# Kernel tuning notes

Measured on AMD Instinct MI355X. Metric: run time of the kernel, lower is better.

## Reference

```python
import jax, jax.numpy as jnp
import numpy as np

B, D, N, C = 4096, 2048, 8, 1024  # batch, in_features, ncomponents, per-component out channels


def setup_inputs() -> dict:
    key = jax.random.key(0)
    k1, k2, k3, k4 = jax.random.split(key, 4)
    scale_w = 1.0 / np.sqrt(D)
    return {
        "x": jax.random.normal(k1, (B, D), dtype=jnp.float32),
        "W": jax.random.normal(k2, (N, C, D), dtype=jnp.float32) * scale_w,
        "b": jax.random.normal(k3, (N, C), dtype=jnp.float32) * scale_w,
        "Wg_w": jax.random.normal(k4, (D, 1), dtype=jnp.float32) * scale_w,
        "Wg_b": jnp.zeros((1,), dtype=jnp.float32),
    }


def reference(x, W, b, Wg_w, Wg_b):
    n = W.shape[0]
    # scalar gate per sample: g in [0, ncomponents]
    g = n * 0.5 * (1.0 + jnp.tanh(x @ Wg_w + Wg_b))            # [B, 1]
    k = jnp.floor(g)                                            # [B, 1]
    idx = jnp.arange(n, dtype=x.dtype)[None, :]                 # [1, N]
    M_hard = (idx <= k).astype(x.dtype)                        # monotonic prefix mask [B, N]
    # straight-through estimator: forward = hard mask, grad wrt g = sum over components
    M = jax.lax.stop_gradient(M_hard - g) + g                   # [B, N]
    # L1 normalize (torch fn.normalize p=1, eps=1e-12)
    G = M / jnp.maximum(jnp.sum(jnp.abs(M), axis=1, keepdims=True), 1e-12)
    # all component outputs; unselected components have G==0 so they contribute the
    # same zeros the original pads with (equal-width components, out = N*C)
    Y = jnp.einsum('bd,ncd->bnc', x, W) + b                     # [B, N, C]
    E = (G[:, :, None] * Y).reshape(x.shape[0], -1)             # [B, N*C]
    return E, G
```

## Files before the change

kernel.cpp:

```cpp
#include <hip/hip_runtime.h>
#include <hip/hip_bf16.h>

#define BATCH 4096
#define DK    2048
#define NCOMP 8
#define CCH   1024
#define NC    8192

typedef unsigned int u32;
typedef unsigned short u16;
typedef short bf16x8 __attribute__((ext_vector_type(8)));
typedef float f32x4 __attribute__((ext_vector_type(4)));

__device__ __forceinline__ u16 f2bf(float f) {
    union { float f; u32 u; } v; v.f = f;
    u32 r = v.u + 0x7fffu + ((v.u >> 16) & 1u);
    return (u16)(r >> 16);
}

__global__ void cvt_kernel(const float* __restrict__ in, u16* __restrict__ out, int n8) {
    int i = blockIdx.x * blockDim.x + threadIdx.x;
    if (i >= n8) return;
    const float4* p = (const float4*)in + (size_t)i * 2;
    float4 a = p[0], b = p[1];
    union { u16 s[8]; uint4 v; } o;
    o.s[0] = f2bf(a.x); o.s[1] = f2bf(a.y); o.s[2] = f2bf(a.z); o.s[3] = f2bf(a.w);
    o.s[4] = f2bf(b.x); o.s[5] = f2bf(b.y); o.s[6] = f2bf(b.z); o.s[7] = f2bf(b.w);
    ((uint4*)out)[i] = o.v;
}

__global__ void gate_kernel(const float* __restrict__ x, const float* __restrict__ wg,
                            const float* __restrict__ wgb, float* __restrict__ Gout) {
    int wid = (int)((blockIdx.x * blockDim.x + threadIdx.x) >> 6);
    int l = threadIdx.x & 63;
    if (wid >= BATCH) return;
    const float4* xr = (const float4*)(x + (size_t)wid * DK);
    const float4* wr = (const float4*)wg;
    float s = 0.f;
#pragma unroll
    for (int j = 0; j < 8; ++j) {
        float4 a = xr[j * 64 + l];
        float4 b = wr[j * 64 + l];
        s += a.x * b.x; s += a.y * b.y; s += a.z * b.z; s += a.w * b.w;
    }
#pragma unroll
    for (int off = 32; off; off >>= 1) s += __shfl_xor(s, off, 64);
    if (l == 0) {
        float g = 0.5f * (float)NCOMP * (1.0f + tanhf(s + wgb[0]));
        float k = floorf(g);
        float mh[NCOMP];
        float den = 0.f;
#pragma unroll
        for (int n = 0; n < NCOMP; ++n) {
            float m = ((float)n <= k) ? 1.0f : 0.0f;
            m = (m - g) + g;
            mh[n] = m;
            den += fabsf(m);
        }
        den = fmaxf(den, 1e-12f);
#pragma unroll
        for (int n = 0; n < NCOMP; ++n) Gout[wid * NCOMP + n] = mh[n] / den;
    }
}

#define BM 128
#define BN 128
#define BKK 32

__global__ __launch_bounds__(256, 2)
void gemm_kernel(const u16* __restrict__ A,
                 const u16* __restrict__ Bw,
                 const float* __restrict__ bias,
                 const float* __restrict__ Gtab,
                 float* __restrict__ E) {
    __shared__ u16 As[BM * BKK];
    __shared__ u16 Bs[BN * BKK];
    int tid = threadIdx.x;
    int w = tid >> 6, l = tid & 63;

    const int nbc = NC / BN;
    const int cpx = (BATCH / BM) * nbc / 8;
    int bid = blockIdx.x;
    int swz = (bid & 7) * cpx + (bid >> 3);
    int brow = (swz / nbc) * BM;
    int bcol = (swz % nbc) * BN;
    int wr = w >> 1, wc = w & 1;

    f32x4 acc[4][4] = {};

    int r0 = tid >> 2, kp0 = (tid & 3) * 8;
    u16* ldsA0 = As + (size_t)(w * 64) * 8;
    u16* ldsA1 = As + (size_t)(256 + w * 64) * 8;
    u16* ldsB0 = Bs + (size_t)(w * 64) * 8;
    u16* ldsB1 = Bs + (size_t)(256 + w * 64) * 8;
    const u16* gA0 = A + (size_t)(brow + r0) * DK + kp0;
    const u16* gA1 = A + (size_t)(brow + r0 + 64) * DK + kp0;
    const u16* gB0 = Bw + (size_t)(bcol + r0) * DK + kp0;
    const u16* gB1 = Bw + (size_t)(bcol + r0 + 64) * DK + kp0;

    int arow = l & 15;
    int kgrp = (l >> 4) * 8;

    for (int k0 = 0; k0 < DK; k0 += BKK) {
        __builtin_amdgcn_global_load_lds((const __attribute__((address_space(1))) u32*)(gA0 + k0),
                                         (__attribute__((address_space(3))) u32*)ldsA0, 16, 0, 0);
        __builtin_amdgcn_global_load_lds((const __attribute__((address_space(1))) u32*)(gA1 + k0),
                                         (__attribute__((address_space(3))) u32*)ldsA1, 16, 0, 0);
        __builtin_amdgcn_global_load_lds((const __attribute__((address_space(1))) u32*)(gB0 + k0),
                                         (__attribute__((address_space(3))) u32*)ldsB0, 16, 0, 0);
        __builtin_amdgcn_global_load_lds((const __attribute__((address_space(1))) u32*)(gB1 + k0),
                                         (__attribute__((address_space(3))) u32*)ldsB1, 16, 0, 0);
        __syncthreads();

        bf16x8 af[4], bf[4];
#pragma unroll
        for (int mi = 0; mi < 4; ++mi)
            af[mi] = *(const bf16x8*)&As[(wr * 64 + mi * 16 + arow) * BKK + kgrp];
#pragma unroll
        for (int ni = 0; ni < 4; ++ni)
            bf[ni] = *(const bf16x8*)&Bs[(wc * 64 + ni * 16 + arow) * BKK + kgrp];
#pragma unroll
        for (int mi = 0; mi < 4; ++mi)
#pragma unroll
            for (int ni = 0; ni < 4; ++ni)
                acc[mi][ni] = __builtin_amdgcn_mfma_f32_16x16x32_bf16(af[mi], bf[ni], acc[mi][ni], 0, 0, 0);
        __syncthreads();
    }

    int n = bcol >> 10;
    int rbase = brow + wr * 64;
    int cbase = bcol + wc * 64;
#pragma unroll
    for (int mi = 0; mi < 4; ++mi) {
#pragma unroll
        for (int r = 0; r < 4; ++r) {
            int row = rbase + mi * 16 + (l >> 4) * 4 + r;
            float gv = Gtab[row * NCOMP + n];
#pragma unroll
            for (int ni = 0; ni < 4; ++ni) {
                int col = cbase + ni * 16 + (l & 15);
                E[(size_t)row * NC + col] = gv * (acc[mi][ni][r] + bias[col]);
            }
        }
    }
}

extern "C" void kernel_launch(void* const* d_in, const int* in_sizes, int n_in,
                              void* d_out, int out_size, void* d_ws, size_t ws_size,
                              hipStream_t stream) {
    const float* x   = (const float*)d_in[0];
    const float* W   = (const float*)d_in[1];
    const float* b   = (const float*)d_in[2];
    const float* wgw = (const float*)d_in[3];
    const float* wgb = (const float*)d_in[4];
    float* E = (float*)d_out;
    float* G = E + (size_t)BATCH * NC;

    u16* xb = (u16*)d_ws;
    u16* Wb = xb + (size_t)BATCH * DK;

    int nx8 = BATCH * DK / 8;
    cvt_kernel<<<nx8 / 256, 256, 0, stream>>>(x, xb, nx8);
    int nw8 = NC * DK / 8;
    cvt_kernel<<<nw8 / 256, 256, 0, stream>>>(W, Wb, nw8);
    gate_kernel<<<BATCH / 4, 256, 0, stream>>>(x, wgw, wgb, G);
    gemm_kernel<<<(BATCH / BM) * (NC / BN), 256, 0, stream>>>(xb, Wb, b, G, E);
}
```

Before: 385.3 us.

## Rewrite GEMM as 256x256 double-buffered swizzled tile and fuse x conversion with gate

The GEMM moves from 128x128x32 tiles with 256 threads to 256x256x64 tiles with 512 threads. LDS is double-buffered and XOR-swizzled, and global-to-LDS prefetch of the next K tile is interleaved with four MFMA phases that raise wave priority. The x bf16 conversion is fused into the gate kernel, so x is read once, and bias is hoisted into registers for the epilogue. The larger tile cuts global traffic per FLOP and the overlap hides load latency, at the cost of much higher register and LDS pressure (128 KB LDS per block with launch bounds of 2 blocks).

```diff
diff --git a/kernel.cpp b/kernel.cpp
--- a/kernel.cpp
+++ b/kernel.cpp
@@ -4,8 +4,8 @@
 #define BATCH 4096
 #define DK    2048
 #define NCOMP 8
-#define CCH   1024
 #define NC    8192
+#define NT    (DK / 64)
 
 typedef unsigned int u32;
 typedef unsigned short u16;
@@ -18,131 +18,209 @@
     return (u16)(r >> 16);
 }
 
-__global__ void cvt_kernel(const float* __restrict__ in, u16* __restrict__ out, int n8) {
+__global__ void cvtW_kernel(const float* __restrict__ in, u16* __restrict__ out) {
     int i = blockIdx.x * blockDim.x + threadIdx.x;
-    if (i >= n8) return;
-    const float4* p = (const float4*)in + (size_t)i * 2;
-    float4 a = p[0], b = p[1];
-    union { u16 s[8]; uint4 v; } o;
-    o.s[0] = f2bf(a.x); o.s[1] = f2bf(a.y); o.s[2] = f2bf(a.z); o.s[3] = f2bf(a.w);
-    o.s[4] = f2bf(b.x); o.s[5] = f2bf(b.y); o.s[6] = f2bf(b.z); o.s[7] = f2bf(b.w);
-    ((uint4*)out)[i] = o.v;
-}
-
-__global__ void gate_kernel(const float* __restrict__ x, const float* __restrict__ wg,
-                            const float* __restrict__ wgb, float* __restrict__ Gout) {
-    int wid = (int)((blockIdx.x * blockDim.x + threadIdx.x) >> 6);
-    int l = threadIdx.x & 63;
-    if (wid >= BATCH) return;
-    const float4* xr = (const float4*)(x + (size_t)wid * DK);
+    float4 a = ((const float4*)in)[i];
+    ushort4 o = { f2bf(a.x), f2bf(a.y), f2bf(a.z), f2bf(a.w) };
+    ((ushort4*)out)[i] = o;
+}
+
+__global__ __launch_bounds__(256)
+void xgate_kernel(const float* __restrict__ x, const float* __restrict__ wg,
+                  const float* __restrict__ wgb, u16* __restrict__ xb,
+                  float* __restrict__ G) {
+    int row = blockIdx.x;
+    int t = threadIdx.x;
+    const float4* xr = (const float4*)(x + (size_t)row * DK);
     const float4* wr = (const float4*)wg;
-    float s = 0.f;
-#pragma unroll
-    for (int j = 0; j < 8; ++j) {
-        float4 a = xr[j * 64 + l];
-        float4 b = wr[j * 64 + l];
-        s += a.x * b.x; s += a.y * b.y; s += a.z * b.z; s += a.w * b.w;
-    }
+    float4 a = xr[t], b = xr[t + 256];
+    float4 wa = wr[t], wb = wr[t + 256];
+    float s = a.x*wa.x + a.y*wa.y + a.z*wa.z + a.w*wa.w
+            + b.x*wb.x + b.y*wb.y + b.z*wb.z + b.w*wb.w;
+    ushort4 o1 = { f2bf(a.x), f2bf(a.y), f2bf(a.z), f2bf(a.w) };
+    ushort4 o2 = { f2bf(b.x), f2bf(b.y), f2bf(b.z), f2bf(b.w) };
+    ushort4* xo = (ushort4*)(xb + (size_t)row * DK);
+    xo[t] = o1;
+    xo[t + 256] = o2;
+    __shared__ float red[4];
 #pragma unroll
     for (int off = 32; off; off >>= 1) s += __shfl_xor(s, off, 64);
-    if (l == 0) {
-        float g = 0.5f * (float)NCOMP * (1.0f + tanhf(s + wgb[0]));
+    if ((t & 63) == 0) red[t >> 6] = s;
+    __syncthreads();
+    if (t == 0) {
+        float sum = (red[0] + red[1]) + (red[2] + red[3]);
+        float g = 0.5f * (float)NCOMP * (1.0f + tanhf(sum + wgb[0]));
         float k = floorf(g);
-        float mh[NCOMP];
-        float den = 0.f;
+        float mh[NCOMP]; float den = 0.f;
 #pragma unroll
         for (int n = 0; n < NCOMP; ++n) {
             float m = ((float)n <= k) ? 1.0f : 0.0f;
             m = (m - g) + g;
-            mh[n] = m;
-            den += fabsf(m);
+            mh[n] = m; den += fabsf(m);
         }
         den = fmaxf(den, 1e-12f);
 #pragma unroll
-        for (int n = 0; n < NCOMP; ++n) Gout[wid * NCOMP + n] = mh[n] / den;
+        for (int n = 0; n < NCOMP; ++n) G[(size_t)row * NCOMP + n] = mh[n] / den;
     }
 }
 
-#define BM 128
-#define BN 128
-#define BKK 32
-
-__global__ __launch_bounds__(256, 2)
-void gemm_kernel(const u16* __restrict__ A,
-                 const u16* __restrict__ Bw,
-                 const float* __restrict__ bias,
-                 const float* __restrict__ Gtab,
+__device__ __forceinline__ void stage_half(const u16* __restrict__ gbase,
+                                           u16* __restrict__ ldsHalf, int tid) {
+#pragma unroll
+    for (int i = 0; i < 2; ++i) {
+        int c = tid + i * 512;
+        int row = c >> 3;
+        int slot = (c & 7) ^ (row & 7);
+        const u16* src = gbase + (size_t)row * DK + slot * 8;
+        u16* dst = ldsHalf + (size_t)(c >> 6) * 512;
+        __builtin_amdgcn_global_load_lds((const __attribute__((address_space(1))) u32*)src,
+                                         (__attribute__((address_space(3))) u32*)dst, 16, 0, 0);
+    }
+}
+
+__device__ __forceinline__ bf16x8 frag(const u16* __restrict__ h, int lrow, int slot) {
+    return *(const bf16x8*)(h + lrow * 64 + ((slot ^ (lrow & 7)) << 3));
+}
+
+#define PH_MID()  do { __builtin_amdgcn_s_barrier(); \
+    asm volatile("s_waitcnt lgkmcnt(0)" ::: "memory"); \
+    __builtin_amdgcn_sched_barrier(0); \
+    __builtin_amdgcn_s_setprio(1); } while (0)
+#define PH_END()  do { __builtin_amdgcn_s_setprio(0); \
+    __builtin_amdgcn_s_barrier(); } while (0)
+
+__global__ __launch_bounds__(512, 2)
+void gemm_kernel(const u16* __restrict__ A, const u16* __restrict__ Bw,
+                 const float* __restrict__ bias, const float* __restrict__ Gtab,
                  float* __restrict__ E) {
-    __shared__ u16 As[BM * BKK];
-    __shared__ u16 Bs[BN * BKK];
+    __shared__ u16 lds[2][2][2][128 * 64];
     int tid = threadIdx.x;
-    int w = tid >> 6, l = tid & 63;
-
-    const int nbc = NC / BN;
-    const int cpx = (BATCH / BM) * nbc / 8;
+    int l = tid & 63;
+    int w = tid >> 6;
+    int wr = w >> 2, wc = w & 3;
+    int r16 = l & 15, kg = l >> 4;
+
     int bid = blockIdx.x;
-    int swz = (bid & 7) * cpx + (bid >> 3);
-    int brow = (swz / nbc) * BM;
-    int bcol = (swz % nbc) * BN;
-    int wr = w >> 1, wc = w & 1;
-
-    f32x4 acc[4][4] = {};
-
-    int r0 = tid >> 2, kp0 = (tid & 3) * 8;
-    u16* ldsA0 = As + (size_t)(w * 64) * 8;
-    u16* ldsA1 = As + (size_t)(256 + w * 64) * 8;
-    u16* ldsB0 = Bs + (size_t)(w * 64) * 8;
-    u16* ldsB1 = Bs + (size_t)(256 + w * 64) * 8;
-    const u16* gA0 = A + (size_t)(brow + r0) * DK + kp0;
-    const u16* gA1 = A + (size_t)(brow + r0 + 64) * DK + kp0;
-    const u16* gB0 = Bw + (size_t)(bcol + r0) * DK + kp0;
-    const u16* gB1 = Bw + (size_t)(bcol + r0 + 64) * DK + kp0;
-
-    int arow = l & 15;
-    int kgrp = (l >> 4) * 8;
-
-    for (int k0 = 0; k0 < DK; k0 += BKK) {
-        __builtin_amdgcn_global_load_lds((const __attribute__((address_space(1))) u32*)(gA0 + k0),
-                                         (__attribute__((address_space(3))) u32*)ldsA0, 16, 0, 0);
-        __builtin_amdgcn_global_load_lds((const __attribute__((address_space(1))) u32*)(gA1 + k0),
-                                         (__attribute__((address_space(3))) u32*)ldsA1, 16, 0, 0);
-        __builtin_amdgcn_global_load_lds((const __attribute__((address_space(1))) u32*)(gB0 + k0),
-                                         (__attribute__((address_space(3))) u32*)ldsB0, 16, 0, 0);
-        __builtin_amdgcn_global_load_lds((const __attribute__((address_space(1))) u32*)(gB1 + k0),
-                                         (__attribute__((address_space(3))) u32*)ldsB1, 16, 0, 0);
-        __syncthreads();
-
-        bf16x8 af[4], bf[4];
-#pragma unroll
-        for (int mi = 0; mi < 4; ++mi)
-            af[mi] = *(const bf16x8*)&As[(wr * 64 + mi * 16 + arow) * BKK + kgrp];
-#pragma unroll
-        for (int ni = 0; ni < 4; ++ni)
-            bf[ni] = *(const bf16x8*)&Bs[(wc * 64 + ni * 16 + arow) * BKK + kgrp];
-#pragma unroll
-        for (int mi = 0; mi < 4; ++mi)
+    int swz = (bid & 7) * 64 + (bid >> 3);
+    int brow = (swz >> 5) * 256;
+    int bcol = (swz & 31) * 256;
+
+    f32x4 acc[8][4] = {};
+
+    const u16* gA = A + (size_t)brow * DK;
+    const u16* gB = Bw + (size_t)bcol * DK;
+
+    stage_half(gA,              lds[0][0][0], tid);
+    stage_half(gA + 128 * DK,   lds[0][0][1], tid);
+    stage_half(gB,              lds[0][1][0], tid);
+    stage_half(gB + 128 * DK,   lds[0][1][1], tid);
+    asm volatile("s_waitcnt vmcnt(0)" ::: "memory");
+    __builtin_amdgcn_s_barrier();
+
+    for (int t = 0; t < NT; ++t) {
+        int buf = t & 1, nb = buf ^ 1;
+        const u16* Ah = lds[buf][0][wr];
+        const u16* Bh = lds[buf][1][wc >> 1];
+        int brB = (wc & 1) * 64;
+        int koff = (t + 1) * 64;
+        bool pf = (t + 1) < NT;
+
+        bf16x8 aF[4][2], bF[2][2];
+#pragma unroll
+        for (int j = 0; j < 4; ++j)
+#pragma unroll
+            for (int kk = 0; kk < 2; ++kk)
+                aF[j][kk] = frag(Ah, j * 16 + r16, kk * 4 + kg);
+#pragma unroll
+        for (int jn = 0; jn < 2; ++jn)
+#pragma unroll
+            for (int kk = 0; kk < 2; ++kk)
+                bF[jn][kk] = frag(Bh, brB + jn * 16 + r16, kk * 4 + kg);
+        if (pf) {
+            stage_half(gA + koff,            lds[nb][0][0], tid);
+            stage_half(gA + 128 * DK + koff, lds[nb][0][1], tid);
+        }
+        PH_MID();
+#pragma unroll
+        for (int j = 0; j < 4; ++j)
+#pragma unroll
+            for (int jn = 0; jn < 2; ++jn)
+#pragma unroll
+                for (int kk = 0; kk < 2; ++kk)
+                    acc[j][jn] = __builtin_amdgcn_mfma_f32_16x16x32_bf16(aF[j][kk], bF[jn][kk], acc[j][jn], 0, 0, 0);
+        PH_END();
+
+        bf16x8 bG[2][2];
+#pragma unroll
+        for (int jn = 0; jn < 2; ++jn)
+#pragma unroll
+            for (int kk = 0; kk < 2; ++kk)
+                bG[jn][kk] = frag(Bh, brB + 32 + jn * 16 + r16, kk * 4 + kg);
+        if (pf) {
+            stage_half(gB + koff,            lds[nb][1][0], tid);
+            stage_half(gB + 128 * DK + koff, lds[nb][1][1], tid);
+        }
+        PH_MID();
+#pragma unroll
+        for (int j = 0; j < 4; ++j)
+#pragma unroll
+            for (int jn = 0; jn < 2; ++jn)
+#pragma unroll
+                for (int kk = 0; kk < 2; ++kk)
+                    acc[j][2 + jn] = __builtin_amdgcn_mfma_f32_16x16x32_bf16(aF[j][kk], bG[jn][kk], acc[j][2 + jn], 0, 0, 0);
+        PH_END();
+
+        bf16x8 aG[4][2];
+#pragma unroll
+        for (int j = 0; j < 4; ++j)
+#pragma unroll
+            for (int kk = 0; kk < 2; ++kk)
+                aG[j][kk] = frag(Ah, 64 + j * 16 + r16, kk * 4 + kg);
+        PH_MID();
+#pragma unroll
+        for (int j = 0; j < 4; ++j)
+#pragma unroll
+            for (int jn = 0; jn < 2; ++jn)
+#pragma unroll
+                for (int kk = 0; kk < 2; ++kk)
+                    acc[4 + j][2 + jn] = __builtin_amdgcn_mfma_f32_16x16x32_bf16(aG[j][kk], bG[jn][kk], acc[4 + j][2 + jn], 0, 0, 0);
+        PH_END();
+
+#pragma unroll
+        for (int jn = 0; jn < 2; ++jn)
+#pragma unroll
+            for (int kk = 0; kk < 2; ++kk)
+                bF[jn][kk] = frag(Bh, brB + jn * 16 + r16, kk * 4 + kg);
+        PH_MID();
+#pragma unroll
+        for (int j = 0; j < 4; ++j)
+#pragma unroll
+            for (int jn = 0; jn < 2; ++jn)
+#pragma unroll
+                for (int kk = 0; kk < 2; ++kk)
+                    acc[4 + j][jn] = __builtin_amdgcn_mfma_f32_16x16x32_bf16(aG[j][kk], bF[jn][kk], acc[4 + j][jn], 0, 0, 0);
+        __builtin_amdgcn_s_setprio(0);
+        if (pf) asm volatile("s_waitcnt vmcnt(0)" ::: "memory");
+        __builtin_amdgcn_s_barrier();
+    }
+
+    int ncomp = (bcol + wc * 64) >> 10;
+    int rbase = brow + wr * 128;
+    int cbase = bcol + wc * 64;
+    float bs[4];
+#pragma unroll
+    for (int ni = 0; ni < 4; ++ni) bs[ni] = bias[cbase + ni * 16 + r16];
+#pragma unroll
+    for (int mi = 0; mi < 8; ++mi)
+#pragma unroll
+        for (int r = 0; r < 4; ++r) {
+            int row = rbase + mi * 16 + kg * 4 + r;
+            float gv = Gtab[(size_t)row * NCOMP + ncomp];
+            float* Erow = E + (size_t)row * NC + cbase;
 #pragma unroll
             for (int ni = 0; ni < 4; ++ni)
-                acc[mi][ni] = __builtin_amdgcn_mfma_f32_16x16x32_bf16(af[mi], bf[ni], acc[mi][ni], 0, 0, 0);
-        __syncthreads();
-    }
-
-    int n = bcol >> 10;
-    int rbase = brow + wr * 64;
-    int cbase = bcol + wc * 64;
-#pragma unroll
-    for (int mi = 0; mi < 4; ++mi) {
-#pragma unroll
-        for (int r = 0; r < 4; ++r) {
-            int row = rbase + mi * 16 + (l >> 4) * 4 + r;
-            float gv = Gtab[row * NCOMP + n];
-#pragma unroll
-            for (int ni = 0; ni < 4; ++ni) {
-                int col = cbase + ni * 16 + (l & 15);
-                E[(size_t)row * NC + col] = gv * (acc[mi][ni][r] + bias[col]);
-            }
-        }
-    }
+                Erow[ni * 16 + r16] = gv * (acc[mi][ni][r] + bs[ni]);
+        }
 }
 
 extern "C" void kernel_launch(void* const* d_in, const int* in_sizes, int n_in,
@@ -159,10 +237,7 @@
     u16* xb = (u16*)d_ws;
     u16* Wb = xb + (size_t)BATCH * DK;
 
-    int nx8 = BATCH * DK / 8;
-    cvt_kernel<<<nx8 / 256, 256, 0, stream>>>(x, xb, nx8);
-    int nw8 = NC * DK / 8;
-    cvt_kernel<<<nw8 / 256, 256, 0, stream>>>(W, Wb, nw8);
-    gate_kernel<<<BATCH / 4, 256, 0, stream>>>(x, wgw, wgb, G);
-    gemm_kernel<<<(BATCH / BM) * (NC / BN), 256, 0, stream>>>(xb, Wb, b, G, E);
-}
+    cvtW_kernel<<<NC * DK / 4 / 256, 256, 0, stream>>>(W, Wb);
+    xgate_kernel<<<BATCH, 256, 0, stream>>>(x, wgw, wgb, xb, G);
+    gemm_kernel<<<(BATCH / 256) * (NC / 256), 512, 0, stream>>>(xb, Wb, b, G, E);
+}
```

New measurement: 327.9 us. -14.9%, faster.
